# Optimization experiments

Hardware: AMD Instinct MI355X
Metric: run time of the kernel (lower is better)

## Reference

```python
import math
import jax, jax.numpy as jnp
import numpy as np

N_HEAD = 32
N_KV_HEADS = 8
HEAD_DIM = 128
N_EMBD = 4096
B, T = 1, 2048


def apply_rope(x, cos, sin):
    # x: [B, H, T, D]; cos/sin: [T, D//2] -> broadcast over B, H
    half = x.shape[-1] // 2
    c = cos[None, None, :, :]
    s = sin[None, None, :, :]
    x1, x2 = x[..., :half], x[..., half:]
    return jnp.concatenate([x1 * c - x2 * s, x2 * c + x1 * s], axis=-1).astype(x.dtype)


def setup_inputs() -> dict:
    key = jax.random.key(0)
    ks = jax.random.split(key, 7)
    x = jax.random.normal(ks[0], (B, T, N_EMBD), dtype=jnp.float32)
    # realistic rope tables
    inv_freq = 1.0 / (10000.0 ** (jnp.arange(0, HEAD_DIM, 2, dtype=jnp.float32) / HEAD_DIM))
    angles = jnp.arange(T, dtype=jnp.float32)[:, None] * inv_freq[None, :]  # [T, D//2]
    rope_cos = jnp.cos(angles)
    rope_sin = jnp.sin(angles)
    sc = 1.0 / math.sqrt(N_EMBD)
    Wq = jax.random.normal(ks[1], (N_EMBD, N_HEAD * HEAD_DIM), dtype=jnp.float32) * sc
    Wk = jax.random.normal(ks[2], (N_EMBD, N_KV_HEADS * HEAD_DIM), dtype=jnp.float32) * sc
    Wv = jax.random.normal(ks[3], (N_EMBD, N_KV_HEADS * HEAD_DIM), dtype=jnp.float32) * sc
    Wo = jax.random.normal(ks[4], (N_HEAD * HEAD_DIM, N_EMBD), dtype=jnp.float32) * sc
    return {"x": x, "rope_cos": rope_cos, "rope_sin": rope_sin,
            "Wq": Wq, "Wk": Wk, "Wv": Wv, "Wo": Wo}


def reference(x, rope_cos, rope_sin, Wq, Wk, Wv, Wo):
    Bx, Tx, _ = x.shape
    n_rep = N_HEAD // N_KV_HEADS
    # QKV projections (no bias, Llama-style) -> [B, H, T, D]
    q = jnp.einsum('btd,df->btf', x, Wq).reshape(Bx, Tx, N_HEAD, HEAD_DIM).transpose(0, 2, 1, 3)
    k = jnp.einsum('btd,df->btf', x, Wk).reshape(Bx, Tx, N_KV_HEADS, HEAD_DIM).transpose(0, 2, 1, 3)
    v = jnp.einsum('btd,df->btf', x, Wv).reshape(Bx, Tx, N_KV_HEADS, HEAD_DIM).transpose(0, 2, 1, 3)
    q = apply_rope(q, rope_cos, rope_sin)
    k = apply_rope(k, rope_cos, rope_sin)
    # GQA: repeat_interleave kv heads to match query heads
    if n_rep > 1:
        k = jnp.repeat(k, n_rep, axis=1)
        v = jnp.repeat(v, n_rep, axis=1)
    scale = 1.0 / math.sqrt(HEAD_DIM)
    scores = jnp.einsum('bhqd,bhkd->bhqk', q, k) * scale  # [B, H, T, T]
    causal = jnp.tril(jnp.ones((Tx, Tx), dtype=bool))
    scores = jnp.where(causal[None, None, :, :], scores, jnp.finfo(scores.dtype).min)
    attn = jax.nn.softmax(scores, axis=-1)
    y = jnp.einsum('bhqk,bhkd->bhqd', attn, v)
    y = y.transpose(0, 2, 1, 3).reshape(Bx, Tx, N_HEAD * HEAD_DIM)
    return jnp.einsum('btf,fd->btd', y, Wo)
```

## Files before the change

### kernel.cpp

```cpp
#include <hip/hip_runtime.h>

typedef unsigned short u16;
typedef __bf16 bf16x8 __attribute__((ext_vector_type(8)));
typedef float f32x4 __attribute__((ext_vector_type(4)));

__device__ __forceinline__ u16 f2bf(float f) {
    unsigned int u = __builtin_bit_cast(unsigned int, f);
    u += 0x7fffu + ((u >> 16) & 1u);
    return (u16)(u >> 16);
}
__device__ __forceinline__ float bf2f(u16 b) {
    unsigned int u = ((unsigned int)b) << 16;
    return __builtin_bit_cast(float, u);
}
__device__ __forceinline__ void load_lds16(const void* g, void* l) {
    __builtin_amdgcn_global_load_lds((__attribute__((address_space(1))) void*)(g),
                                     (__attribute__((address_space(3))) void*)(l), 16, 0, 0);
}
__device__ __forceinline__ f32x4 mfma16(bf16x8 a, bf16x8 b, f32x4 c) {
    return __builtin_amdgcn_mfma_f32_16x16x32_bf16(a, b, c, 0, 0, 0);
}

__global__ __launch_bounds__(256) void k_cvt_bf16(const float* __restrict__ in,
                                                  u16* __restrict__ out, int n4) {
    int i = blockIdx.x * 256 + threadIdx.x;
    if (i < n4) {
        float4 v = ((const float4*)in)[i];
        unsigned int lo = (unsigned int)f2bf(v.x) | ((unsigned int)f2bf(v.y) << 16);
        unsigned int hi = (unsigned int)f2bf(v.z) | ((unsigned int)f2bf(v.w) << 16);
        ((uint2*)out)[i] = make_uint2(lo, hi);
    }
}

__global__ __launch_bounds__(256) void k_transpose_cvt(const float* __restrict__ W,
                                                       u16* __restrict__ Wt, int K, int N) {
    __shared__ u16 t[32][33];
    int tx = threadIdx.x & 31, ty = threadIdx.x >> 5;
    int n0 = blockIdx.x * 32, k0 = blockIdx.y * 32;
#pragma unroll
    for (int i = 0; i < 4; i++)
        t[ty + i * 8][tx] = f2bf(W[(size_t)(k0 + ty + i * 8) * N + n0 + tx]);
    __syncthreads();
#pragma unroll
    for (int i = 0; i < 4; i++)
        Wt[(size_t)(n0 + ty + i * 8) * K + k0 + tx] = t[tx][ty + i * 8];
}

__global__ __launch_bounds__(256) void k_transpose_v(const u16* __restrict__ KV,
                                                     u16* __restrict__ Vt) {
    __shared__ u16 t[32][33];
    int tx = threadIdx.x & 31, ty = threadIdx.x >> 5;
    int t0 = blockIdx.x * 32, d0 = blockIdx.y * 32, kh = blockIdx.z;
#pragma unroll
    for (int i = 0; i < 4; i++)
        t[ty + i * 8][tx] = KV[(size_t)(t0 + ty + i * 8) * 2048 + 1024 + kh * 128 + d0 + tx];
    __syncthreads();
#pragma unroll
    for (int i = 0; i < 4; i++)
        Vt[((size_t)kh * 128 + d0 + ty + i * 8) * 2048 + t0 + tx] = t[tx][ty + i * 8];
}

__global__ __launch_bounds__(256) void k_rope(u16* __restrict__ X,
                                              const float* __restrict__ cosT,
                                              const float* __restrict__ sinT, int nheads,
                                              int rowstride) {
    int idx = blockIdx.x * 256 + threadIdx.x;
    int d = idx & 63;
    int h = (idx >> 6) & (nheads - 1);
    int tp = idx / (nheads * 64);
    size_t base = (size_t)tp * rowstride + h * 128 + d;
    float q1 = bf2f(X[base]), q2 = bf2f(X[base + 64]);
    float c = cosT[tp * 64 + d], s = sinT[tp * 64 + d];
    X[base] = f2bf(q1 * c - q2 * s);
    X[base + 64] = f2bf(q2 * c + q1 * s);
}

template <typename OutT>
__global__ __launch_bounds__(256) void k_gemm_bt(const u16* __restrict__ A,
                                                 const u16* __restrict__ B,
                                                 OutT* __restrict__ C, int M, int N, int K) {
    __shared__ u16 sA[128 * 32];
    __shared__ u16 sB[128 * 32];
    const int tid = threadIdx.x;
    const int wave = tid >> 6, lane = tid & 63;
    const int m0 = blockIdx.y << 7, n0 = blockIdx.x << 7;
    const int wr = (wave >> 1) << 6, wc = (wave & 1) << 6;
    const int r0 = tid >> 2;
    const int kb = (tid & 3) << 4;
    const int fr = lane & 15;
    const int fkb = (lane >> 4) << 4;

    f32x4 acc[4][4] = {};
    const char* gA = (const char*)A + ((size_t)(m0 + r0) * K) * 2 + kb;
    const char* gB = (const char*)B + ((size_t)(n0 + r0) * K) * 2 + kb;
    char* lA = (char*)sA + wave * 1024;
    char* lB = (char*)sB + wave * 1024;
    const size_t rowskip = (size_t)64 * K * 2;

    for (int k0 = 0; k0 < K; k0 += 32) {
        load_lds16(gA, lA);
        load_lds16(gA + rowskip, lA + 4096);
        load_lds16(gB, lB);
        load_lds16(gB + rowskip, lB + 4096);
        gA += 64; gB += 64;
        __syncthreads();
        bf16x8 af[4], bg[4];
#pragma unroll
        for (int i = 0; i < 4; i++)
            af[i] = *(const bf16x8*)((const char*)sA + ((wr + i * 16 + fr) << 6) + fkb);
#pragma unroll
        for (int j = 0; j < 4; j++)
            bg[j] = *(const bf16x8*)((const char*)sB + ((wc + j * 16 + fr) << 6) + fkb);
#pragma unroll
        for (int i = 0; i < 4; i++)
#pragma unroll
            for (int j = 0; j < 4; j++)
                acc[i][j] = mfma16(af[i], bg[j], acc[i][j]);
        __syncthreads();
    }
    const int rr = (lane >> 4) << 2, cc = lane & 15;
#pragma unroll
    for (int i = 0; i < 4; i++)
#pragma unroll
        for (int j = 0; j < 4; j++)
#pragma unroll
            for (int r = 0; r < 4; r++) {
                float v = acc[i][j][r];
                OutT sv;
                if constexpr (sizeof(OutT) == 2) sv = f2bf(v); else sv = v;
                C[(size_t)(m0 + wr + i * 16 + rr + r) * N + (n0 + wc + j * 16 + cc)] = sv;
            }
}

__global__ __launch_bounds__(256, 2) void k_attn(const u16* __restrict__ Q,
                                                 const u16* __restrict__ K,
                                                 const u16* __restrict__ Vt,
                                                 u16* __restrict__ Y) {
    __shared__ u16 kt[64 * 128];
    __shared__ u16 vt[128 * 64];
    __shared__ u16 pl[4 * 16 * 64];
    const int tid = threadIdx.x;
    const int wave = tid >> 6, lane = tid & 63;
    const int l15 = lane & 15, l4 = lane >> 4;
    const int h = blockIdx.y, kh = h >> 2;
    const float scale = 0.08838834764831845f;

    char* ktb = (char*)kt;
    char* vtb = (char*)vt;
    char* plb = (char*)pl + wave * 2048;

#pragma unroll 1
    for (int qsel = 0; qsel < 2; qsel++) {
        const int qt = qsel == 0 ? blockIdx.x : 31 - blockIdx.x;
        const int qw = qt * 64 + wave * 16;

        bf16x8 aq[4];
#pragma unroll
        for (int kf = 0; kf < 4; kf++)
            aq[kf] = *(const bf16x8*)(Q + (size_t)(qw + l15) * 4096 + h * 128 + kf * 32 + l4 * 8);

        f32x4 o[8] = {};
        float mrow[4], lrow[4];
#pragma unroll
        for (int rg = 0; rg < 4; rg++) { mrow[rg] = -1e30f; lrow[rg] = 0.f; }

        const int nkt = qt + 1;
        for (int it = 0; it < nkt; ++it) {
            const int kbase = it << 6;
#pragma unroll
            for (int p = 0; p < 4; p++) {
                int ol = wave * 4096 + p * 1024 + lane * 16;
                int key = ol >> 8, db = ol & 255;
                int src = db ^ ((key & 7) << 4);
                load_lds16((const char*)K + ((size_t)(kbase + key) * 2048 + kh * 128) * 2 + src,
                           ktb + wave * 4096 + p * 1024);
            }
#pragma unroll
            for (int p = 0; p < 4; p++) {
                int ol = wave * 4096 + p * 1024 + lane * 16;
                int d = ol >> 7, kb2 = ol & 127;
                int src = kb2 ^ ((d & 7) << 4);
                load_lds16((const char*)Vt + ((size_t)(kh * 128 + d) * 2048 + kbase) * 2 + src,
                           vtb + wave * 4096 + p * 1024);
            }
            __syncthreads();

            f32x4 s[4];
#pragma unroll
            for (int tc = 0; tc < 4; tc++) {
                bf16x8 bk[4];
                const int key = tc * 16 + l15;
                const int swz = (key & 7) << 4;
#pragma unroll
                for (int kf = 0; kf < 4; kf++)
                    bk[kf] = *(const bf16x8*)(ktb + key * 256 + ((kf * 64 + l4 * 16) ^ swz));
                f32x4 sv = {0.f, 0.f, 0.f, 0.f};
#pragma unroll
                for (int kf = 0; kf < 4; kf++) sv = mfma16(aq[kf], bk[kf], sv);
                s[tc] = sv;
            }
#pragma unroll
            for (int rg = 0; rg < 4; rg++) {
                const int qrow = qw + l4 * 4 + rg;
                float mx = -1e30f;
#pragma unroll
                for (int tc = 0; tc < 4; tc++) {
                    float v = s[tc][rg] * scale;
                    int key = kbase + tc * 16 + l15;
                    v = (key > qrow) ? -1e30f : v;
                    s[tc][rg] = v;
                    mx = fmaxf(mx, v);
                }
                mx = fmaxf(mx, __shfl_xor(mx, 1));
                mx = fmaxf(mx, __shfl_xor(mx, 2));
                mx = fmaxf(mx, __shfl_xor(mx, 4));
                mx = fmaxf(mx, __shfl_xor(mx, 8));
                const float mold = mrow[rg];
                const float mnew = fmaxf(mold, mx);
                const float corr = __expf(mold - mnew);
                mrow[rg] = mnew;
                float rs = 0.f;
#pragma unroll
                for (int tc = 0; tc < 4; tc++) {
                    float p = __expf(s[tc][rg] - mnew);
                    s[tc][rg] = p;
                    rs += p;
                }
                rs += __shfl_xor(rs, 1);
                rs += __shfl_xor(rs, 2);
                rs += __shfl_xor(rs, 4);
                rs += __shfl_xor(rs, 8);
                lrow[rg] = lrow[rg] * corr + rs;
#pragma unroll
                for (int dc = 0; dc < 8; dc++) o[dc][rg] *= corr;
            }
#pragma unroll
            for (int rg = 0; rg < 4; rg++) {
                const int row = l4 * 4 + rg;
                const int swz = (row & 7) << 4;
#pragma unroll
                for (int tc = 0; tc < 4; tc++) {
                    const int cb = (tc * 16 + l15) * 2;
                    *(u16*)(plb + row * 128 + (cb ^ swz)) = f2bf(s[tc][rg]);
                }
            }
            bf16x8 pa[2];
            {
                const int row = l15;
                const int swz = (row & 7) << 4;
#pragma unroll
                for (int kf = 0; kf < 2; kf++)
                    pa[kf] = *(const bf16x8*)(plb + row * 128 + ((kf * 64 + l4 * 16) ^ swz));
            }
#pragma unroll
            for (int dc = 0; dc < 8; dc++) {
                bf16x8 vf[2];
                const int d = dc * 16 + l15;
                const int swz = (d & 7) << 4;
#pragma unroll
                for (int kf = 0; kf < 2; kf++)
                    vf[kf] = *(const bf16x8*)(vtb + d * 128 + ((kf * 64 + l4 * 16) ^ swz));
                o[dc] = mfma16(pa[0], vf[0], o[dc]);
                o[dc] = mfma16(pa[1], vf[1], o[dc]);
            }
            __syncthreads();
        }
#pragma unroll
        for (int rg = 0; rg < 4; rg++) {
            const float inv = 1.f / lrow[rg];
            const int row = qw + l4 * 4 + rg;
#pragma unroll
            for (int dc = 0; dc < 8; dc++)
                Y[(size_t)row * 4096 + h * 128 + dc * 16 + l15] = f2bf(o[dc][rg] * inv);
        }
        __syncthreads();
    }
}

extern "C" void kernel_launch(void* const* d_in, const int* in_sizes, int n_in,
                              void* d_out, int out_size, void* d_ws, size_t ws_size,
                              hipStream_t stream) {
    const float* x  = (const float*)d_in[0];
    const float* rc = (const float*)d_in[1];
    const float* rs = (const float*)d_in[2];
    const float* Wq = (const float*)d_in[3];
    const float* Wk = (const float*)d_in[4];
    const float* Wv = (const float*)d_in[5];
    const float* Wo = (const float*)d_in[6];
    float* out = (float*)d_out;

    char* ws = (char*)d_ws;
    u16* xb  = (u16*)(ws);
    u16* Wt  = (u16*)(ws + 16777216);
    u16* Qb  = (u16*)(ws + 50331648);
    u16* KV  = (u16*)(ws + 67108864);
    u16* Vtb = (u16*)(ws + 75497472);
    u16* Y   = (u16*)(ws + 79691776);

    k_cvt_bf16<<<8192, 256, 0, stream>>>(x, xb, 2097152);
    k_transpose_cvt<<<dim3(128, 128), 256, 0, stream>>>(Wq, Wt, 4096, 4096);
    k_gemm_bt<u16><<<dim3(32, 16), 256, 0, stream>>>(xb, Wt, Qb, 2048, 4096, 4096);
    k_transpose_cvt<<<dim3(32, 128), 256, 0, stream>>>(Wk, Wt, 4096, 1024);
    k_transpose_cvt<<<dim3(32, 128), 256, 0, stream>>>(Wv, Wt + (size_t)1024 * 4096, 4096, 1024);
    k_gemm_bt<u16><<<dim3(16, 16), 256, 0, stream>>>(xb, Wt, KV, 2048, 2048, 4096);
    k_rope<<<16384, 256, 0, stream>>>(Qb, rc, rs, 32, 4096);
    k_rope<<<4096, 256, 0, stream>>>(KV, rc, rs, 8, 2048);
    k_transpose_v<<<dim3(64, 4, 8), 256, 0, stream>>>(KV, Vtb);
    k_attn<<<dim3(16, 32), 256, 0, stream>>>(Qb, KV, Vtb, Y);
    k_transpose_cvt<<<dim3(128, 128), 256, 0, stream>>>(Wo, Wt, 4096, 4096);
    k_gemm_bt<float><<<dim3(32, 16), 256, 0, stream>>>(Y, Wt, out, 2048, 4096, 4096);
}
```

Before: 626.1 us.

## Fuse Q/K/V projections into one GEMM, merge RoPE, add XCD-aware block swizzle

Concatenates the transposed Wq, Wk and Wv into a single 6144-wide weight matrix so one GEMM produces a packed QKV buffer. The two RoPE launches become one kernel, and the attention and V-transpose kernels now index the shared 6144 row stride. The GEMM also remaps block IDs so consecutive tiles land on the same XCD, which should improve L2 reuse. Together these cut launch count and the tail of the smaller KV GEMM. The trade-off is a larger strided QKV buffer, plus Y now reuses the xb workspace region.

```diff
diff --git a/kernel.cpp b/kernel.cpp
--- a/kernel.cpp
+++ b/kernel.cpp
@@ -46,33 +46,33 @@
         Wt[(size_t)(n0 + ty + i * 8) * K + k0 + tx] = t[tx][ty + i * 8];
 }
 
-__global__ __launch_bounds__(256) void k_transpose_v(const u16* __restrict__ KV,
+__global__ __launch_bounds__(256) void k_transpose_v(const u16* __restrict__ QKV,
                                                      u16* __restrict__ Vt) {
     __shared__ u16 t[32][33];
     int tx = threadIdx.x & 31, ty = threadIdx.x >> 5;
     int t0 = blockIdx.x * 32, d0 = blockIdx.y * 32, kh = blockIdx.z;
 #pragma unroll
     for (int i = 0; i < 4; i++)
-        t[ty + i * 8][tx] = KV[(size_t)(t0 + ty + i * 8) * 2048 + 1024 + kh * 128 + d0 + tx];
+        t[ty + i * 8][tx] = QKV[(size_t)(t0 + ty + i * 8) * 6144 + 5120 + kh * 128 + d0 + tx];
     __syncthreads();
 #pragma unroll
     for (int i = 0; i < 4; i++)
         Vt[((size_t)kh * 128 + d0 + ty + i * 8) * 2048 + t0 + tx] = t[tx][ty + i * 8];
 }
 
-__global__ __launch_bounds__(256) void k_rope(u16* __restrict__ X,
-                                              const float* __restrict__ cosT,
-                                              const float* __restrict__ sinT, int nheads,
-                                              int rowstride) {
+__global__ __launch_bounds__(256) void k_rope2(u16* __restrict__ QKV,
+                                               const float* __restrict__ cosT,
+                                               const float* __restrict__ sinT) {
     int idx = blockIdx.x * 256 + threadIdx.x;
     int d = idx & 63;
-    int h = (idx >> 6) & (nheads - 1);
-    int tp = idx / (nheads * 64);
-    size_t base = (size_t)tp * rowstride + h * 128 + d;
-    float q1 = bf2f(X[base]), q2 = bf2f(X[base + 64]);
+    int h = (idx >> 6) % 40;
+    int tp = idx / (40 * 64);
+    int col = h < 32 ? h * 128 : 4096 + (h - 32) * 128;
+    size_t base = (size_t)tp * 6144 + col + d;
+    float q1 = bf2f(QKV[base]), q2 = bf2f(QKV[base + 64]);
     float c = cosT[tp * 64 + d], s = sinT[tp * 64 + d];
-    X[base] = f2bf(q1 * c - q2 * s);
-    X[base + 64] = f2bf(q2 * c + q1 * s);
+    QKV[base] = f2bf(q1 * c - q2 * s);
+    QKV[base + 64] = f2bf(q2 * c + q1 * s);
 }
 
 template <typename OutT>
@@ -83,7 +83,14 @@
     __shared__ u16 sB[128 * 32];
     const int tid = threadIdx.x;
     const int wave = tid >> 6, lane = tid & 63;
-    const int m0 = blockIdx.y << 7, n0 = blockIdx.x << 7;
+    const int gx = (int)gridDim.x;
+    const int nwg = gx * (int)gridDim.y;
+    const int orig = (int)blockIdx.y * gx + (int)blockIdx.x;
+    const int qq = nwg >> 3, rr8 = nwg & 7;
+    const int xcd = orig & 7, bidx = orig >> 3;
+    const int swz = (xcd < rr8 ? xcd * (qq + 1) : rr8 * (qq + 1) + (xcd - rr8) * qq) + bidx;
+    const int m0 = (swz / gx) << 7;
+    const int n0 = (swz % gx) << 7;
     const int wr = (wave >> 1) << 6, wc = (wave & 1) << 6;
     const int r0 = tid >> 2;
     const int kb = (tid & 3) << 4;
@@ -157,7 +164,7 @@
         bf16x8 aq[4];
 #pragma unroll
         for (int kf = 0; kf < 4; kf++)
-            aq[kf] = *(const bf16x8*)(Q + (size_t)(qw + l15) * 4096 + h * 128 + kf * 32 + l4 * 8);
+            aq[kf] = *(const bf16x8*)(Q + (size_t)(qw + l15) * 6144 + h * 128 + kf * 32 + l4 * 8);
 
         f32x4 o[8] = {};
         float mrow[4], lrow[4];
@@ -172,7 +179,7 @@
                 int ol = wave * 4096 + p * 1024 + lane * 16;
                 int key = ol >> 8, db = ol & 255;
                 int src = db ^ ((key & 7) << 4);
-                load_lds16((const char*)K + ((size_t)(kbase + key) * 2048 + kh * 128) * 2 + src,
+                load_lds16((const char*)K + ((size_t)(kbase + key) * 6144 + kh * 128) * 2 + src,
                            ktb + wave * 4096 + p * 1024);
             }
 #pragma unroll
@@ -292,21 +299,18 @@
     char* ws = (char*)d_ws;
     u16* xb  = (u16*)(ws);
     u16* Wt  = (u16*)(ws + 16777216);
-    u16* Qb  = (u16*)(ws + 50331648);
-    u16* KV  = (u16*)(ws + 67108864);
-    u16* Vtb = (u16*)(ws + 75497472);
-    u16* Y   = (u16*)(ws + 79691776);
+    u16* QKV = (u16*)(ws + 67108864);
+    u16* Vtb = (u16*)(ws + 92274688);
+    u16* Y   = xb;
 
     k_cvt_bf16<<<8192, 256, 0, stream>>>(x, xb, 2097152);
     k_transpose_cvt<<<dim3(128, 128), 256, 0, stream>>>(Wq, Wt, 4096, 4096);
-    k_gemm_bt<u16><<<dim3(32, 16), 256, 0, stream>>>(xb, Wt, Qb, 2048, 4096, 4096);
-    k_transpose_cvt<<<dim3(32, 128), 256, 0, stream>>>(Wk, Wt, 4096, 1024);
-    k_transpose_cvt<<<dim3(32, 128), 256, 0, stream>>>(Wv, Wt + (size_t)1024 * 4096, 4096, 1024);
-    k_gemm_bt<u16><<<dim3(16, 16), 256, 0, stream>>>(xb, Wt, KV, 2048, 2048, 4096);
-    k_rope<<<16384, 256, 0, stream>>>(Qb, rc, rs, 32, 4096);
-    k_rope<<<4096, 256, 0, stream>>>(KV, rc, rs, 8, 2048);
-    k_transpose_v<<<dim3(64, 4, 8), 256, 0, stream>>>(KV, Vtb);
-    k_attn<<<dim3(16, 32), 256, 0, stream>>>(Qb, KV, Vtb, Y);
+    k_transpose_cvt<<<dim3(32, 128), 256, 0, stream>>>(Wk, Wt + (size_t)4096 * 4096, 4096, 1024);
+    k_transpose_cvt<<<dim3(32, 128), 256, 0, stream>>>(Wv, Wt + (size_t)5120 * 4096, 4096, 1024);
+    k_gemm_bt<u16><<<dim3(48, 16), 256, 0, stream>>>(xb, Wt, QKV, 2048, 6144, 4096);
+    k_rope2<<<20480, 256, 0, stream>>>(QKV, rc, rs);
+    k_transpose_v<<<dim3(64, 4, 8), 256, 0, stream>>>(QKV, Vtb);
+    k_attn<<<dim3(16, 32), 256, 0, stream>>>(QKV, QKV + 4096, Vtb, Y);
     k_transpose_cvt<<<dim3(128, 128), 256, 0, stream>>>(Wo, Wt, 4096, 4096);
     k_gemm_bt<float><<<dim3(32, 16), 256, 0, stream>>>(Y, Wt, out, 2048, 4096, 4096);
 }
```

Measured after the change: 570.4 us. 8.9% less time.
